# Optimization experiments

Measured on AMD Instinct MI355X. Metric: run time of the kernel, lower is better.

Reference implementation:

```python
import jax, jax.numpy as jnp
import numpy as np

NHEAD = 16


def setup_inputs() -> dict:
    key = jax.random.key(0)
    ks = jax.random.split(key, 9)
    d = 1024
    scale = 0.03  # keep projected q,k in a sane range (like trained weights)
    return {
        "x": jax.random.normal(ks[0], (4, 4096, d), jnp.float32),
        "wq": jax.random.normal(ks[1], (d, d), jnp.float32) * scale,
        "bq": jax.random.normal(ks[2], (d,), jnp.float32) * scale,
        "wk": jax.random.normal(ks[3], (d, d), jnp.float32) * scale,
        "bk": jax.random.normal(ks[4], (d,), jnp.float32) * scale,
        "wv": jax.random.normal(ks[5], (d, d), jnp.float32) * scale,
        "bv": jax.random.normal(ks[6], (d,), jnp.float32) * scale,
        "wo": jax.random.normal(ks[7], (d, d), jnp.float32) * scale,
        "bo": jax.random.normal(ks[8], (d,), jnp.float32) * scale,
        "window_size": 128,
    }


def reference(x, wq, bq, wk, bk, wv, bv, wo, bo, window_size):
    B, S, D = x.shape
    H = NHEAD
    Dh = D // H
    w = int(window_size)

    def proj(wm, b):
        # [B,S,D] -> [B,H,S,Dh]
        return (x @ wm.T + b).reshape(B, S, H, Dh).transpose(0, 2, 1, 3)

    q = proj(wq, bq)
    k = proj(wk, bk)
    v = proj(wv, bv)

    # Pad K/V along seq so offset slices are static-size [B,H,S,Dh].
    Kp = jnp.pad(k, ((0, 0), (0, 0), (w, w), (0, 0)))
    Vp = jnp.pad(v, ((0, 0), (0, 0), (w, w), (0, 0)))
    pos = jnp.arange(S)
    inv_sqrt = np.float32(1.0 / np.sqrt(Dh))

    # Faithful to the Triton kernel: a sequential scan over window offsets with a
    # RUNNING max but NO rescaling of the accumulators (the kernel's exact math).
    def step(carry, t):
        m, o_acc, t_acc = carry
        kj = jax.lax.dynamic_slice_in_dim(Kp, t, S, axis=2)  # key at offset t-w
        vj = jax.lax.dynamic_slice_in_dim(Vp, t, S, axis=2)
        s = jnp.einsum("bhsd,bhsd->bhs", q, kj) * inv_sqrt
        j = pos + t - w
        valid = (j >= 0) & (j < S)  # [S], broadcasts over [B,H,S]
        m_new = jnp.where(valid, jnp.maximum(m, s), m)
        p = jnp.exp(jnp.where(valid, s - m_new, -jnp.inf))  # 0 where invalid
        return (m_new, o_acc + p[..., None] * vj, t_acc + p), None

    init = (
        jnp.full((B, H, S), -jnp.inf, dtype=x.dtype),
        jnp.zeros((B, H, S, Dh), dtype=x.dtype),
        jnp.zeros((B, H, S), dtype=x.dtype),
    )
    (m, o_acc, t_acc), _ = jax.lax.scan(step, init, jnp.arange(2 * w + 1))
    o = o_acc / t_acc[..., None]  # [B,H,S,Dh]
    out = o.transpose(0, 2, 1, 3).reshape(B, S, D)
    return out @ wo.T + bo
```

## Files before the change

kernel.cpp:

```cpp
#include <hip/hip_runtime.h>
#include <math.h>

#define S_LEN  4096
#define BATCH  4
#define DMODEL 1024
#define NHEADS 16
#define DHEAD  64
#define WIN    128

typedef _Float16 half8   __attribute__((ext_vector_type(8)));
typedef _Float16 half4_t __attribute__((ext_vector_type(4)));
typedef float    floatx4 __attribute__((ext_vector_type(4)));

__device__ __forceinline__ void gload16(const void* g, void* l) {
    __builtin_amdgcn_global_load_lds(
        (const __attribute__((address_space(1))) void*)g,
        (__attribute__((address_space(3))) void*)l, 16, 0, 0);
}

__global__ __launch_bounds__(256)
void cvt5_f32_f16(const float4* __restrict__ x,  half4_t* __restrict__ xo, int n4x,
                  const float4* __restrict__ w0, const float4* __restrict__ w1,
                  const float4* __restrict__ w2, const float4* __restrict__ w3,
                  half4_t* __restrict__ o0, half4_t* __restrict__ o1,
                  half4_t* __restrict__ o2, half4_t* __restrict__ o3, int n4w) {
    const int y = blockIdx.y;
    const float4* in  = y == 0 ? x  : (y == 1 ? w0 : (y == 2 ? w1 : (y == 3 ? w2 : w3)));
    half4_t*      out = y == 0 ? xo : (y == 1 ? o0 : (y == 2 ? o1 : (y == 3 ? o2 : o3)));
    const int n4 = y == 0 ? n4x : n4w;
    for (int i = blockIdx.x * blockDim.x + threadIdx.x; i < n4;
         i += gridDim.x * blockDim.x) {
        const float4 a = in[i];
        half4_t h;
        h[0] = (_Float16)a.x; h[1] = (_Float16)a.y;
        h[2] = (_Float16)a.z; h[3] = (_Float16)a.w;
        out[i] = h;
    }
}

template<int MODE, int NTN>
__global__ __launch_bounds__(256)
void gemm2b(const _Float16* __restrict__ A, const _Float16* __restrict__ W,
            const float* __restrict__ B0, const float* __restrict__ B1,
            const float* __restrict__ B2, void* __restrict__ out_base)
{
    constexpr int K  = DMODEL;
    constexpr int nt = K / 64;
    const int bid  = blockIdx.x;
    const int nwg8 = (128 * NTN) >> 3;
    const int swz  = (bid & 7) * nwg8 + (bid >> 3);
    const int i0   = (swz / NTN) * 128;
    const int n0   = (swz % NTN) * 128;

    __shared__ _Float16 As[4][64 * 64];
    __shared__ _Float16 Bs[4][64 * 64];

    const int tid  = threadIdx.x;
    const int lane = tid & 63;
    const int wid  = tid >> 6;
    const int wr   = wid >> 1;
    const int wc   = wid & 1;
    const int fr   = lane & 15;
    const int fh   = lane >> 4;
    const int sw8  = fr & 7;
    const int ok0  = ((fh) ^ sw8) * 8;
    const int ok1  = ((4 + fh) ^ sw8) * 8;
    const int frow = fr * 64;

    const int srow = tid >> 3;
    const int ssw  = ((tid & 7) ^ (srow & 7)) << 3;
    const _Float16* baseA = A + (size_t)(i0 + srow) * K + ssw;
    const _Float16* baseB = W + (size_t)(n0 + srow) * K + ssw;
    const int ldso = tid * 8;

    floatx4 acc[4][4];
    #pragma unroll
    for (int mi = 0; mi < 4; ++mi)
        #pragma unroll
        for (int ni = 0; ni < 4; ++ni) acc[mi][ni] = (floatx4)0.f;

    half8 a[4][2], b[4][2];

#define ST_A(TT, H)                                                          \
    do {                                                                     \
        _Float16* d_ = &As[(((TT) & 1) << 1) | (H)][ldso];                   \
        const _Float16* s_ = baseA + (size_t)((H) * 64) * K + (TT) * 64;     \
        gload16(s_, d_);                                                     \
        gload16(s_ + (size_t)32 * K, d_ + 2048);                             \
    } while (0)
#define ST_B(TT, H)                                                          \
    do {                                                                     \
        _Float16* d_ = &Bs[(((TT) & 1) << 1) | (H)][ldso];                   \
        const _Float16* s_ = baseB + (size_t)((H) * 64) * K + (TT) * 64;     \
        gload16(s_, d_);                                                     \
        gload16(s_ + (size_t)32 * K, d_ + 2048);                             \
    } while (0)

    ST_A(0, 0); ST_B(0, 0); ST_A(0, 1); ST_B(0, 1);
    ST_A(1, 0); ST_B(1, 0); ST_A(1, 1); ST_B(1, 1);
    asm volatile("s_waitcnt vmcnt(8)" ::: "memory");
    __builtin_amdgcn_sched_barrier(0);
    __builtin_amdgcn_s_barrier();

    for (int t = 0; t < nt; ++t) {
        const int d2 = (t & 1) << 1;
        const bool st = (t + 2) < nt;

        #pragma unroll
        for (int mi = 0; mi < 4; ++mi) {
            a[mi][0] = *(const half8*)&As[d2 | wr][mi * 1024 + frow + ok0];
            a[mi][1] = *(const half8*)&As[d2 | wr][mi * 1024 + frow + ok1];
        }
        #pragma unroll
        for (int ni = 0; ni < 4; ++ni) {
            b[ni][0] = *(const half8*)&Bs[d2 | wc][ni * 1024 + frow + ok0];
            b[ni][1] = *(const half8*)&Bs[d2 | wc][ni * 1024 + frow + ok1];
        }
        asm volatile("s_waitcnt lgkmcnt(0)" ::: "memory");
        __builtin_amdgcn_sched_barrier(0);
        __builtin_amdgcn_s_barrier();

        if (st) { ST_A(t + 2, 0); ST_B(t + 2, 0); ST_A(t + 2, 1); ST_B(t + 2, 1); }

        __builtin_amdgcn_s_setprio(1);
        #pragma unroll
        for (int kc = 0; kc < 2; ++kc)
            #pragma unroll
            for (int mi = 0; mi < 4; ++mi)
                #pragma unroll
                for (int ni = 0; ni < 4; ++ni)
                    acc[mi][ni] = __builtin_amdgcn_mfma_f32_16x16x32_f16(
                        a[mi][kc], b[ni][kc], acc[mi][ni], 0, 0, 0);
        __builtin_amdgcn_s_setprio(0);

        if (st) {
            asm volatile("s_waitcnt vmcnt(8)" ::: "memory");
        } else if (t + 1 < nt) {
            asm volatile("s_waitcnt vmcnt(0)" ::: "memory");
        }
        __builtin_amdgcn_sched_barrier(0);
        __builtin_amdgcn_s_barrier();
    }
#undef ST_A
#undef ST_B

    const int r0 = (lane >> 4) * 4;
    const int z  = (MODE == 0) ? (n0 >> 10) : 0;
    const float* bz = (MODE == 1) ? B0 : (z == 0 ? B0 : (z == 1 ? B1 : B2));

    #pragma unroll
    for (int ni = 0; ni < 4; ++ni) {
        const int gc   = n0 + wc * 64 + ni * 16 + fr;
        const int gcol = gc & (DMODEL - 1);
        const float bv = bz[gcol];
        #pragma unroll
        for (int mi = 0; mi < 4; ++mi) {
            const int gr = i0 + wr * 64 + mi * 16 + r0;
            const floatx4 v = acc[mi][ni];
            if (MODE == 0) {
                _Float16* outh = (_Float16*)out_base
                               + (size_t)z * ((size_t)16384 * DMODEL);
                const int bb = gr >> 12;
                const int sp = gr & (S_LEN - 1);
                const int hh = gcol >> 6;
                const int dh = gcol & 63;
                if (z < 2) {
                    #pragma unroll
                    for (int r = 0; r < 4; ++r)
                        outh[((((size_t)(bb * NHEADS + hh)) * S_LEN + sp + r) << 6) + dh] =
                            (_Float16)(v[r] + bv);
                } else {
                    half4_t hv;
                    hv[0] = (_Float16)(v[0] + bv); hv[1] = (_Float16)(v[1] + bv);
                    hv[2] = (_Float16)(v[2] + bv); hv[3] = (_Float16)(v[3] + bv);
                    *(half4_t*)&outh[(((size_t)(bb * NHEADS + hh)) * DHEAD + dh) * S_LEN + sp] = hv;
                }
            } else {
                float* out = (float*)out_base;
                #pragma unroll
                for (int r = 0; r < 4; ++r)
                    out[(size_t)(gr + r) * DMODEL + gcol] = v[r] + bv;
            }
        }
    }
}

__global__ __launch_bounds__(256)
void attn_mfma(const _Float16* __restrict__ qh_, const _Float16* __restrict__ kh_,
               const _Float16* __restrict__ vth_, _Float16* __restrict__ o)
{
    __shared__ __align__(16) _Float16 Qs[64 * 64];
    __shared__ __align__(16) _Float16 Ks[64 * 64];
    __shared__ __align__(16) _Float16 Vt[64 * 64];
    __shared__ __align__(16) float    SP[64 * 68];
    __shared__ __align__(16) _Float16 P16[64 * 64];
    __shared__ float TqL[64];

    const int tid   = threadIdx.x;
    const int lane  = tid & 63;
    const int w     = tid >> 6;
    const int qbase = blockIdx.x * 64;
    const int head  = blockIdx.y, b = blockIdx.z;
    const size_t bh = (size_t)(b * NHEADS + head);

    const _Float16* qg = qh_  + bh * (size_t)(S_LEN * DHEAD);
    const _Float16* kg = kh_  + bh * (size_t)(S_LEN * DHEAD);
    const _Float16* vg = vth_ + bh * (size_t)(DHEAD * S_LEN);

    const int fr  = lane & 15;
    const int fh  = lane >> 4;
    const int sqt = 16 * w + (lane >> 2);
    const int sg  = lane & 3;
    const int gb  = lane & ~3;

    #pragma unroll
    for (int rep = 0; rep < 2; ++rep) {
        const int c = tid + 256 * rep;
        const int row = c >> 3, sll = c & 7;
        gload16(qg + (size_t)(qbase + row) * 64 + (size_t)((sll ^ (row & 7)) * 8),
                Qs + (size_t)c * 8);
    }

    float mq = -INFINITY;
    float tq = 0.f;

    floatx4 Oacc[4];
    #pragma unroll
    for (int ni = 0; ni < 4; ++ni) Oacc[ni] = (floatx4)0.f;

    for (int c = 0; c < 5; ++c) {
        const int jlo = qbase - WIN + c * 64;
        if (jlo < 0 || jlo >= S_LEN) continue;
        const int base_rel = jlo - qbase + WIN;

        __syncthreads();

        #pragma unroll
        for (int rep = 0; rep < 2; ++rep) {
            const int cc = tid + 256 * rep;
            const int row = cc >> 3, sll = cc & 7;
            gload16(kg + (size_t)(jlo + row) * 64 + (size_t)((sll ^ (row & 7)) * 8),
                    Ks + (size_t)cc * 8);
            gload16(vg + (size_t)row * S_LEN + jlo + (size_t)((sll ^ (row & 7)) * 8),
                    Vt + (size_t)cc * 8);
        }
        __syncthreads();

        {
            floatx4 acc[4];
            #pragma unroll
            for (int ni = 0; ni < 4; ++ni) acc[ni] = (floatx4)0.f;
            half8 a[2];
            #pragma unroll
            for (int kc = 0; kc < 2; ++kc) {
                const int row = 16 * w + fr;
                a[kc] = *(const half8*)&Qs[row * 64 + ((fh + 4 * kc) ^ (row & 7)) * 8];
            }
            #pragma unroll
            for (int ni = 0; ni < 4; ++ni)
                #pragma unroll
                for (int kc = 0; kc < 2; ++kc) {
                    const int tr = 16 * ni + fr;
                    half8 bf = *(const half8*)&Ks[tr * 64 + ((fh + 4 * kc) ^ (tr & 7)) * 8];
                    acc[ni] = __builtin_amdgcn_mfma_f32_16x16x32_f16(a[kc], bf, acc[ni], 0, 0, 0);
                }
            #pragma unroll
            for (int ni = 0; ni < 4; ++ni)
                #pragma unroll
                for (int r = 0; r < 4; ++r)
                    SP[(16 * w + 4 * fh + r) * 68 + fr + 16 * ni] = acc[ni][r] * 0.125f;
        }
        asm volatile("s_waitcnt lgkmcnt(0)" ::: "memory");
        __builtin_amdgcn_sched_barrier(0);

        {
            float sv[16], run[16];
            float m_run = -INFINITY;
            #pragma unroll
            for (int u = 0; u < 4; ++u) {
                const float4 s4 = *(const float4*)&SP[sqt * 68 + sg * 16 + 4 * u];
                const float se[4] = {s4.x, s4.y, s4.z, s4.w};
                #pragma unroll
                for (int e = 0; e < 4; ++e) {
                    const int i = 4 * u + e;
                    const int rel = base_rel + sg * 16 + i - sqt;
                    const bool valid = (rel >= 0) && (rel <= 2 * WIN);
                    const float s = valid ? se[e] : -INFINITY;
                    sv[i] = s;
                    m_run = fmaxf(m_run, s);
                    run[i] = m_run;
                }
            }
            const float cm = m_run;
            const float c0 = __shfl(cm, gb + 0);
            const float c1 = __shfl(cm, gb + 1);
            const float c2 = __shfl(cm, gb + 2);
            const float c3 = __shfl(cm, gb + 3);
            float pre = mq;
            if (sg > 0) pre = fmaxf(pre, c0);
            if (sg > 1) pre = fmaxf(pre, c1);
            if (sg > 2) pre = fmaxf(pre, c2);

            float tl = 0.f;
            _Float16 pf[16];
            #pragma unroll
            for (int i = 0; i < 16; ++i) {
                const float wm = fmaxf(pre, run[i]);
                const float p = (sv[i] != -INFINITY) ? __expf(sv[i] - wm) : 0.f;
                tl += p;
                pf[i] = (_Float16)p;
            }
            #pragma unroll
            for (int u = 0; u < 2; ++u) {
                half8 h8;
                #pragma unroll
                for (int e = 0; e < 8; ++e) h8[e] = pf[8 * u + e];
                *(half8*)&P16[sqt * 64 + ((2 * sg + u) ^ (sqt & 7)) * 8] = h8;
            }
            const float t0 = __shfl(tl, gb + 0);
            const float t1 = __shfl(tl, gb + 1);
            const float t2 = __shfl(tl, gb + 2);
            const float t3 = __shfl(tl, gb + 3);
            tq += t0 + t1 + t2 + t3;
            mq = fmaxf(mq, fmaxf(fmaxf(c0, c1), fmaxf(c2, c3)));
        }
        asm volatile("s_waitcnt lgkmcnt(0)" ::: "memory");
        __builtin_amdgcn_sched_barrier(0);

        {
            half8 pa[2];
            #pragma unroll
            for (int kc = 0; kc < 2; ++kc) {
                const int row = 16 * w + fr;
                pa[kc] = *(const half8*)&P16[row * 64 + ((fh + 4 * kc) ^ (row & 7)) * 8];
            }
            #pragma unroll
            for (int ni = 0; ni < 4; ++ni)
                #pragma unroll
                for (int kc = 0; kc < 2; ++kc) {
                    const int dr = 16 * ni + fr;
                    half8 bf = *(const half8*)&Vt[dr * 64 + ((fh + 4 * kc) ^ (dr & 7)) * 8];
                    Oacc[ni] = __builtin_amdgcn_mfma_f32_16x16x32_f16(pa[kc], bf, Oacc[ni], 0, 0, 0);
                }
        }
    }

    if (sg == 0) TqL[sqt] = tq;
    asm volatile("s_waitcnt lgkmcnt(0)" ::: "memory");
    __builtin_amdgcn_sched_barrier(0);

    #pragma unroll
    for (int ni = 0; ni < 4; ++ni)
        #pragma unroll
        for (int r = 0; r < 4; ++r) {
            const int q  = 16 * w + 4 * fh + r;
            const float inv = 1.0f / TqL[q];
            o[((size_t)(b * S_LEN + qbase + q) * NHEADS + head) * DHEAD + fr + 16 * ni] =
                (_Float16)(Oacc[ni][r] * inv);
        }
}

extern "C" void kernel_launch(void* const* d_in, const int* in_sizes, int n_in,
                              void* d_out, int out_size, void* d_ws, size_t ws_size,
                              hipStream_t stream) {
    const float* x  = (const float*)d_in[0];
    const float* wq = (const float*)d_in[1];
    const float* bq = (const float*)d_in[2];
    const float* wk = (const float*)d_in[3];
    const float* bk = (const float*)d_in[4];
    const float* wv = (const float*)d_in[5];
    const float* bv = (const float*)d_in[6];
    const float* wo = (const float*)d_in[7];
    const float* bo = (const float*)d_in[8];

    const size_t BUF = (size_t)BATCH * S_LEN * DMODEL;
    _Float16* xh  = (_Float16*)d_ws;
    _Float16* qh  = xh + BUF;
    _Float16* kh  = qh + BUF;
    _Float16* vth = kh + BUF;
    _Float16* oh  = vth + BUF;
    _Float16* wqh = oh + BUF;
    _Float16* wkh = wqh + DMODEL * DMODEL;
    _Float16* wvh = wkh + DMODEL * DMODEL;
    _Float16* woh = wvh + DMODEL * DMODEL;

    cvt5_f32_f16<<<dim3(512, 5), 256, 0, stream>>>(
        (const float4*)x, (half4_t*)xh, (int)(BUF / 4),
        (const float4*)wq, (const float4*)wk, (const float4*)wv, (const float4*)wo,
        (half4_t*)wqh, (half4_t*)wkh, (half4_t*)wvh, (half4_t*)woh,
        DMODEL * DMODEL / 4);

    gemm2b<0, 24><<<128 * 24, 256, 0, stream>>>(xh, wqh, bq, bk, bv, (void*)qh);

    dim3 gattn(S_LEN / 64, NHEADS, BATCH);
    attn_mfma<<<gattn, 256, 0, stream>>>(qh, kh, vth, oh);

    gemm2b<1, 8><<<128 * 8, 256, 0, stream>>>(oh, woh, bo, bo, bo, d_out);
}
```

Measured before the change: 278.5 us.

## Split GEMM tiles across 8 waves with 512-thread blocks

The projection and output GEMMs now launch 512 threads per 128x128 tile instead of 256. Each of the 8 waves computes a 32x64 sub-tile, which halves the accumulator and A-fragment registers per wave, and launch bounds of (512,4) ask for higher occupancy. Shared memory is re-laid out into two full 128x64 buffers per operand, so each wave reads a slice of them. The cost is that each wave does fewer MFMAs per LDS read, so the ratio of shared-memory traffic to compute rises and barriers synchronize more waves.

```diff
diff --git a/kernel.cpp b/kernel.cpp
--- a/kernel.cpp
+++ b/kernel.cpp
@@ -39,10 +39,10 @@
 }
 
 template<int MODE, int NTN>
-__global__ __launch_bounds__(256)
-void gemm2b(const _Float16* __restrict__ A, const _Float16* __restrict__ W,
-            const float* __restrict__ B0, const float* __restrict__ B1,
-            const float* __restrict__ B2, void* __restrict__ out_base)
+__global__ __launch_bounds__(512, 4)
+void gemm_occ(const _Float16* __restrict__ A, const _Float16* __restrict__ W,
+              const float* __restrict__ B0, const float* __restrict__ B1,
+              const float* __restrict__ B2, void* __restrict__ out_base)
 {
     constexpr int K  = DMODEL;
     constexpr int nt = K / 64;
@@ -52,8 +52,8 @@
     const int i0   = (swz / NTN) * 128;
     const int n0   = (swz % NTN) * 128;
 
-    __shared__ _Float16 As[4][64 * 64];
-    __shared__ _Float16 Bs[4][64 * 64];
+    __shared__ _Float16 As[2][128 * 64];
+    __shared__ _Float16 Bs[2][128 * 64];
 
     const int tid  = threadIdx.x;
     const int lane = tid & 63;
@@ -65,7 +65,8 @@
     const int sw8  = fr & 7;
     const int ok0  = ((fh) ^ sw8) * 8;
     const int ok1  = ((4 + fh) ^ sw8) * 8;
-    const int frow = fr * 64;
+    const int arow = (wr * 32 + fr) * 64;
+    const int brow = (wc * 64 + fr) * 64;
 
     const int srow = tid >> 3;
     const int ssw  = ((tid & 7) ^ (srow & 7)) << 3;
@@ -73,60 +74,57 @@
     const _Float16* baseB = W + (size_t)(n0 + srow) * K + ssw;
     const int ldso = tid * 8;
 
-    floatx4 acc[4][4];
-    #pragma unroll
-    for (int mi = 0; mi < 4; ++mi)
+    floatx4 acc[2][4];
+    #pragma unroll
+    for (int mi = 0; mi < 2; ++mi)
         #pragma unroll
         for (int ni = 0; ni < 4; ++ni) acc[mi][ni] = (floatx4)0.f;
 
-    half8 a[4][2], b[4][2];
-
-#define ST_A(TT, H)                                                          \
+    half8 a[2][2], b[4][2];
+
+#define ST_AB(TT)                                                            \
     do {                                                                     \
-        _Float16* d_ = &As[(((TT) & 1) << 1) | (H)][ldso];                   \
-        const _Float16* s_ = baseA + (size_t)((H) * 64) * K + (TT) * 64;     \
-        gload16(s_, d_);                                                     \
-        gload16(s_ + (size_t)32 * K, d_ + 2048);                             \
+        _Float16* dA = &As[(TT) & 1][ldso];                                  \
+        _Float16* dB = &Bs[(TT) & 1][ldso];                                  \
+        const _Float16* sA = baseA + (TT) * 64;                              \
+        const _Float16* sB = baseB + (TT) * 64;                              \
+        gload16(sA, dA);                                                     \
+        gload16(sA + (size_t)64 * K, dA + 4096);                             \
+        gload16(sB, dB);                                                     \
+        gload16(sB + (size_t)64 * K, dB + 4096);                             \
     } while (0)
-#define ST_B(TT, H)                                                          \
-    do {                                                                     \
-        _Float16* d_ = &Bs[(((TT) & 1) << 1) | (H)][ldso];                   \
-        const _Float16* s_ = baseB + (size_t)((H) * 64) * K + (TT) * 64;     \
-        gload16(s_, d_);                                                     \
-        gload16(s_ + (size_t)32 * K, d_ + 2048);                             \
-    } while (0)
-
-    ST_A(0, 0); ST_B(0, 0); ST_A(0, 1); ST_B(0, 1);
-    ST_A(1, 0); ST_B(1, 0); ST_A(1, 1); ST_B(1, 1);
-    asm volatile("s_waitcnt vmcnt(8)" ::: "memory");
+
+    ST_AB(0);
+    ST_AB(1);
+    asm volatile("s_waitcnt vmcnt(4)" ::: "memory");
     __builtin_amdgcn_sched_barrier(0);
     __builtin_amdgcn_s_barrier();
 
     for (int t = 0; t < nt; ++t) {
-        const int d2 = (t & 1) << 1;
+        const int d = t & 1;
         const bool st = (t + 2) < nt;
 
         #pragma unroll
-        for (int mi = 0; mi < 4; ++mi) {
-            a[mi][0] = *(const half8*)&As[d2 | wr][mi * 1024 + frow + ok0];
-            a[mi][1] = *(const half8*)&As[d2 | wr][mi * 1024 + frow + ok1];
+        for (int mi = 0; mi < 2; ++mi) {
+            a[mi][0] = *(const half8*)&As[d][arow + mi * 1024 + ok0];
+            a[mi][1] = *(const half8*)&As[d][arow + mi * 1024 + ok1];
         }
         #pragma unroll
         for (int ni = 0; ni < 4; ++ni) {
-            b[ni][0] = *(const half8*)&Bs[d2 | wc][ni * 1024 + frow + ok0];
-            b[ni][1] = *(const half8*)&Bs[d2 | wc][ni * 1024 + frow + ok1];
+            b[ni][0] = *(const half8*)&Bs[d][brow + ni * 1024 + ok0];
+            b[ni][1] = *(const half8*)&Bs[d][brow + ni * 1024 + ok1];
         }
         asm volatile("s_waitcnt lgkmcnt(0)" ::: "memory");
         __builtin_amdgcn_sched_barrier(0);
         __builtin_amdgcn_s_barrier();
 
-        if (st) { ST_A(t + 2, 0); ST_B(t + 2, 0); ST_A(t + 2, 1); ST_B(t + 2, 1); }
+        if (st) ST_AB(t + 2);
 
         __builtin_amdgcn_s_setprio(1);
         #pragma unroll
         for (int kc = 0; kc < 2; ++kc)
             #pragma unroll
-            for (int mi = 0; mi < 4; ++mi)
+            for (int mi = 0; mi < 2; ++mi)
                 #pragma unroll
                 for (int ni = 0; ni < 4; ++ni)
                     acc[mi][ni] = __builtin_amdgcn_mfma_f32_16x16x32_f16(
@@ -134,15 +132,14 @@
         __builtin_amdgcn_s_setprio(0);
 
         if (st) {
-            asm volatile("s_waitcnt vmcnt(8)" ::: "memory");
+            asm volatile("s_waitcnt vmcnt(4)" ::: "memory");
         } else if (t + 1 < nt) {
             asm volatile("s_waitcnt vmcnt(0)" ::: "memory");
         }
         __builtin_amdgcn_sched_barrier(0);
         __builtin_amdgcn_s_barrier();
     }
-#undef ST_A
-#undef ST_B
+#undef ST_AB
 
     const int r0 = (lane >> 4) * 4;
     const int z  = (MODE == 0) ? (n0 >> 10) : 0;
@@ -154,8 +151,8 @@
         const int gcol = gc & (DMODEL - 1);
         const float bv = bz[gcol];
         #pragma unroll
-        for (int mi = 0; mi < 4; ++mi) {
-            const int gr = i0 + wr * 64 + mi * 16 + r0;
+        for (int mi = 0; mi < 2; ++mi) {
+            const int gr = i0 + wr * 32 + mi * 16 + r0;
             const floatx4 v = acc[mi][ni];
             if (MODE == 0) {
                 _Float16* outh = (_Float16*)out_base
@@ -390,10 +387,10 @@
         (half4_t*)wqh, (half4_t*)wkh, (half4_t*)wvh, (half4_t*)woh,
         DMODEL * DMODEL / 4);
 
-    gemm2b<0, 24><<<128 * 24, 256, 0, stream>>>(xh, wqh, bq, bk, bv, (void*)qh);
+    gemm_occ<0, 24><<<128 * 24, 512, 0, stream>>>(xh, wqh, bq, bk, bv, (void*)qh);
 
     dim3 gattn(S_LEN / 64, NHEADS, BATCH);
     attn_mfma<<<gattn, 256, 0, stream>>>(qh, kh, vth, oh);
 
-    gemm2b<1, 8><<<128 * 8, 256, 0, stream>>>(oh, woh, bo, bo, bo, d_out);
-}
+    gemm_occ<1, 8><<<128 * 8, 512, 0, stream>>>(oh, woh, bo, bo, bo, d_out);
+}
```

Result: no change. 278.5 us (+0.0%).
